# Optimization experiments

Measured on AMD Instinct MI355X. Metric: run time of the kernel, lower is better.

## Reference

```python
import jax, jax.numpy as jnp
import numpy as np

N = 50000          # node_num
E = 800000         # edges before self-loops (avg degree 16)
H = 1              # heads
C = 64             # out_channel (== embedding dim)
D_IN = 64          # in_channel
NEG_SLOPE = 0.2    # GraphLayer leaky_relu negative_slope
BN_EPS = 1e-5


def setup_inputs() -> dict:
    key = jax.random.key(0)
    ks = jax.random.split(key, 12)
    x = jax.random.normal(ks[0], (N, D_IN), jnp.float32)
    # random edges with no self-loops (forward removes then re-adds self-loops)
    src = jax.random.randint(ks[1], (E,), 0, N, dtype=jnp.int32)
    off = jax.random.randint(ks[2], (E,), 1, N, dtype=jnp.int32)
    dst = (src + off) % N
    edge_index = jnp.stack([src, dst])            # [2, E], row0=j (source), row1=i (target)
    embedding = jax.random.normal(ks[3], (N, C), jnp.float32)
    sc = 1.0 / np.sqrt(D_IN)
    W = jax.random.normal(ks[4], (H * C, D_IN), jnp.float32) * sc   # lin.weight
    att_i = jax.random.normal(ks[5], (1, H, C), jnp.float32) * 0.1
    att_j = jax.random.normal(ks[6], (1, H, C), jnp.float32) * 0.1
    att_em_i = jax.random.normal(ks[7], (1, H, C), jnp.float32) * 0.1
    att_em_j = jax.random.normal(ks[8], (1, H, C), jnp.float32) * 0.1
    bias = jnp.zeros((C,), jnp.float32)           # GraphLayer bias (concat=False)
    bn_gamma = jnp.ones((C,), jnp.float32)
    bn_beta = jnp.zeros((C,), jnp.float32)
    return {"x": x, "edge_index": edge_index, "embedding": embedding, "W": W,
            "att_i": att_i, "att_j": att_j, "att_em_i": att_em_i, "att_em_j": att_em_j,
            "bias": bias, "bn_gamma": bn_gamma, "bn_beta": bn_beta}


def reference(x, edge_index, embedding, W, att_i, att_j, att_em_i, att_em_j, bias, bn_gamma, bn_beta):
    n = x.shape[0]
    xl = (x @ W.T).reshape(n, H, C)                       # lin(x) -> [N, H, C]
    # add self-loops (input edges have none)
    loops = jnp.arange(n, dtype=edge_index.dtype)
    src = jnp.concatenate([edge_index[0], loops])         # j
    dst = jnp.concatenate([edge_index[1], loops])         # i (aggregation target)
    x_j = xl[src]                                         # [E', H, C]
    x_i = xl[dst]
    emb_i = embedding[dst][:, None, :]                    # [E', 1, C] broadcast over heads
    emb_j = embedding[src][:, None, :]
    # alpha = <cat(x_i, emb_i), cat(att_i, att_em_i)> + <cat(x_j, emb_j), cat(att_j, att_em_j)>
    a = ((x_i * att_i).sum(-1) + (emb_i * att_em_i).sum(-1)
         + (x_j * att_j).sum(-1) + (emb_j * att_em_j).sum(-1))   # [E', H]
    a = jnp.where(a >= 0, a, NEG_SLOPE * a)               # leaky_relu(0.2)
    # segment softmax over target nodes
    amax = jax.ops.segment_max(a, dst, num_segments=n)    # every node has a self-loop
    ea = jnp.exp(a - amax[dst])
    denom = jax.ops.segment_sum(ea, dst, num_segments=n)
    alpha = ea / (denom[dst] + 1e-16)                     # [E', H]
    msg = x_j * alpha[..., None]                          # [E', H, C]
    out = jax.ops.segment_sum(msg, dst, num_segments=n)   # [N, H, C]
    out = out.mean(axis=1) + bias                         # concat=False -> head mean
    # BatchNorm1d (training mode: batch stats) + ReLU
    mu = out.mean(axis=0)
    var = ((out - mu) ** 2).mean(axis=0)
    out = (out - mu) * jax.lax.rsqrt(var + BN_EPS) * bn_gamma + bn_beta
    return jnp.maximum(out, 0.0)
```

## Files before the change

### kernel.cpp

```cpp
#include <hip/hip_runtime.h>
#include <hip/hip_bf16.h>

#define NEG_SLOPE 0.2f
#define BN_EPS 1e-5f
#define CAP 48
#define OWNMAX 768

typedef __attribute__((ext_vector_type(8))) short bf16x8;
typedef __attribute__((ext_vector_type(4))) float f32x4;

__device__ __forceinline__ bf16x8 pk8(float4 a, float4 b) {
    union { __hip_bfloat16 h; short s; } u;
    bf16x8 r;
    u.h = __float2bfloat16(a.x); r[0] = u.s;
    u.h = __float2bfloat16(a.y); r[1] = u.s;
    u.h = __float2bfloat16(a.z); r[2] = u.s;
    u.h = __float2bfloat16(a.w); r[3] = u.s;
    u.h = __float2bfloat16(b.x); r[4] = u.s;
    u.h = __float2bfloat16(b.y); r[5] = u.s;
    u.h = __float2bfloat16(b.z); r[6] = u.s;
    u.h = __float2bfloat16(b.w); r[7] = u.s;
    return r;
}

__global__ void __launch_bounds__(256, 4)
k_scatter_mfma(const float* __restrict__ x, const float* __restrict__ W,
               const float* __restrict__ emb,
               const float* __restrict__ att_i, const float* __restrict__ att_j,
               const float* __restrict__ att_em_i, const float* __restrict__ att_em_j,
               const int* __restrict__ src, const int* __restrict__ dst, int E,
               int* __restrict__ cursor, unsigned short* __restrict__ bucket,
               __hip_bfloat16* __restrict__ xlh, float* __restrict__ s_i,
               float* __restrict__ s_j, int N) {
    __shared__ int nown;
    __shared__ int ownidx[OWNMAX];
    {
        int myx = blockIdx.x & 7;
        int slice = blockIdx.x >> 3;
        int per = (E + 255) / 256;
        int e0 = slice * per;
        int e1 = e0 + per; if (e1 > E) e1 = E;
        if (threadIdx.x == 0) nown = 0;
        __syncthreads();
        for (int e = e0 + threadIdx.x; e < e1; e += 256) {
            int d = dst[e];
            if (((d >> 6) & 7) == myx) {
                int k = atomicAdd(&nown, 1);
                if (k < OWNMAX) ownidx[k] = e;
            }
        }
        __syncthreads();
        int n = nown < OWNMAX ? nown : OWNMAX;
        for (int k = threadIdx.x; k < n; k += 256) {
            int e = ownidx[k];
            int d = dst[e];
            int p = atomicAdd(&cursor[d], 1);
            if (p < CAP) bucket[(size_t)d * CAP + p] = (unsigned short)src[e];
        }
    }

    int gw = blockIdx.x * 4 + (threadIdx.x >> 6);
    int ntiles = (N + 15) >> 4;
    if (gw >= ntiles) return;
    int lane = threadIdx.x & 63;
    int m = lane & 15;
    int q = lane >> 4;
    int r0 = gw * 16;

    const float* xrow = x + (size_t)(r0 + m) * 64;
    float4 xa0 = *(const float4*)(xrow + q * 8);
    float4 xa1 = *(const float4*)(xrow + q * 8 + 4);
    float4 xb0 = *(const float4*)(xrow + 32 + q * 8);
    float4 xb1 = *(const float4*)(xrow + 32 + q * 8 + 4);
    bf16x8 A0 = pk8(xa0, xa1);
    bf16x8 A1 = pk8(xb0, xb1);

    f32x4 acc0 = {0.f, 0.f, 0.f, 0.f}, acc1 = acc0, acc2 = acc0, acc3 = acc0;
#define CTILE(ct, accv) { \
        const float* wrow = W + (size_t)(ct * 16 + m) * 64; \
        float4 wb0 = *(const float4*)(wrow + q * 8); \
        float4 wb1 = *(const float4*)(wrow + q * 8 + 4); \
        float4 wb2 = *(const float4*)(wrow + 32 + q * 8); \
        float4 wb3 = *(const float4*)(wrow + 32 + q * 8 + 4); \
        bf16x8 B0 = pk8(wb0, wb1); \
        bf16x8 B1 = pk8(wb2, wb3); \
        accv = __builtin_amdgcn_mfma_f32_16x16x32_bf16(A0, B0, accv, 0, 0, 0); \
        accv = __builtin_amdgcn_mfma_f32_16x16x32_bf16(A1, B1, accv, 0, 0, 0); }
    CTILE(0, acc0) CTILE(1, acc1) CTILE(2, acc2) CTILE(3, acc3)
#undef CTILE

    float ati0 = att_i[m],    ati1 = att_i[16 + m],    ati2 = att_i[32 + m],    ati3 = att_i[48 + m];
    float atj0 = att_j[m],    atj1 = att_j[16 + m],    atj2 = att_j[32 + m],    atj3 = att_j[48 + m];
    float aei0 = att_em_i[m], aei1 = att_em_i[16 + m], aei2 = att_em_i[32 + m], aei3 = att_em_i[48 + m];
    float aej0 = att_em_j[m], aej1 = att_em_j[16 + m], aej2 = att_em_j[32 + m], aej3 = att_em_j[48 + m];
#pragma unroll
    for (int reg = 0; reg < 4; ++reg) {
        int r = r0 + q * 4 + reg;
        if (r < N) {
            float v0 = acc0[reg], v1 = acc1[reg], v2 = acc2[reg], v3 = acc3[reg];
            __hip_bfloat16* xo = xlh + (size_t)r * 64 + m;
            xo[0]  = __float2bfloat16(v0);
            xo[16] = __float2bfloat16(v1);
            xo[32] = __float2bfloat16(v2);
            xo[48] = __float2bfloat16(v3);
            const float* er = emb + (size_t)r * 64 + m;
            float e0 = er[0], e1 = er[16], e2 = er[32], e3 = er[48];
            float pi = v0 * ati0 + v1 * ati1 + v2 * ati2 + v3 * ati3
                     + e0 * aei0 + e1 * aei1 + e2 * aei2 + e3 * aei3;
            float pj = v0 * atj0 + v1 * atj1 + v2 * atj2 + v3 * atj3
                     + e0 * aej0 + e1 * aej1 + e2 * aej2 + e3 * aej3;
#pragma unroll
            for (int o = 1; o < 16; o <<= 1) {
                pi += __shfl_xor(pi, o, 64);
                pj += __shfl_xor(pj, o, 64);
            }
            if (m == 0) { s_i[r] = pi; s_j[r] = pj; }
        }
    }
}

__global__ void __launch_bounds__(256, 8)
k_aggregate(const __hip_bfloat16* __restrict__ xlh, const float* __restrict__ s_i,
            const float* __restrict__ s_j, const int* __restrict__ cursor,
            const unsigned short* __restrict__ bucket, const float* __restrict__ bias,
            __hip_bfloat16* __restrict__ preh, int N) {
    int lane = threadIdx.x & 63;
    int w = threadIdx.x >> 6;
    int i = blockIdx.x * 4 + w;
    if (i >= N) return;

    int deg = cursor[i];
    deg = deg < CAP ? deg : CAP;
    size_t base = (size_t)i * CAP;
    float sii = s_i[i];
    float a_self = sii + s_j[i];
    a_self = a_self >= 0.f ? a_self : NEG_SLOPE * a_self;

    int jreg = 0;
    float areg = -1e30f;
    if (lane < deg) {
        jreg = (int)bucket[base + lane];
        float a = sii + s_j[jreg];
        areg = a >= 0.f ? a : NEG_SLOPE * a;
    }
    float mx = fmaxf(a_self, areg);
#pragma unroll
    for (int o = 32; o; o >>= 1) mx = fmaxf(mx, __shfl_xor(mx, o, 64));
    float wreg = (lane < deg) ? __expf(areg - mx) : 0.f;
    float dsum = wreg;
#pragma unroll
    for (int o = 32; o; o >>= 1) dsum += __shfl_xor(dsum, o, 64);
    float w_self = __expf(a_self - mx);
    float denom = dsum + w_self + 1e-16f;

    float acc = w_self * (float)xlh[(size_t)i * 64 + lane];
    int wbits = __float_as_int(wreg);
    int e = 0;
#define GL(k) int j##k = __builtin_amdgcn_readlane(jreg, e + k); \
              float u##k = __int_as_float(__builtin_amdgcn_readlane(wbits, e + k)); \
              float v##k = (float)xlh[(size_t)j##k * 64 + lane];
#define FM(k) acc = fmaf(u##k, v##k, acc);
    for (; e + 15 < deg; e += 16) {
        GL(0) GL(1) GL(2) GL(3) GL(4) GL(5) GL(6) GL(7)
        GL(8) GL(9) GL(10) GL(11) GL(12) GL(13) GL(14) GL(15)
        FM(0) FM(1) FM(2) FM(3) FM(4) FM(5) FM(6) FM(7)
        FM(8) FM(9) FM(10) FM(11) FM(12) FM(13) FM(14) FM(15)
    }
    for (; e + 7 < deg; e += 8) {
        GL(0) GL(1) GL(2) GL(3) GL(4) GL(5) GL(6) GL(7)
        FM(0) FM(1) FM(2) FM(3) FM(4) FM(5) FM(6) FM(7)
    }
#undef GL
#undef FM
    for (; e < deg; ++e) {
        int j = __builtin_amdgcn_readlane(jreg, e);
        float wv = __int_as_float(__builtin_amdgcn_readlane(wbits, e));
        acc = fmaf(wv, (float)xlh[(size_t)j * 64 + lane], acc);
    }
    preh[(size_t)i * 64 + lane] = __float2bfloat16(acc / denom + bias[lane]);
}

__global__ void k_stats(const __hip_bfloat16* __restrict__ preh, int N,
                        float* __restrict__ sums) {
    int lane = threadIdx.x & 63, w = threadIdx.x >> 6;
    int gwave = blockIdx.x * (blockDim.x >> 6) + w;
    int stride = gridDim.x * (blockDim.x >> 6);
    float s = 0.f, q = 0.f;
    for (int r = gwave; r < N; r += stride) {
        float v = (float)preh[(size_t)r * 64 + lane];
        s += v;
        q = fmaf(v, v, q);
    }
    __shared__ float ls[4][64], lq[4][64];
    ls[w][lane] = s;
    lq[w][lane] = q;
    __syncthreads();
    if (w == 0) {
        s = ls[0][lane] + ls[1][lane] + ls[2][lane] + ls[3][lane];
        q = lq[0][lane] + lq[1][lane] + lq[2][lane] + lq[3][lane];
        atomicAdd(&sums[lane], s);
        atomicAdd(&sums[64 + lane], q);
    }
}

__global__ void __launch_bounds__(256, 4)
k_norm(const __hip_bfloat16* __restrict__ preh, const float* __restrict__ sums,
       const float* __restrict__ gamma, const float* __restrict__ beta,
       float* __restrict__ out, int N, int total4) {
    __shared__ float sc_sh[64], sh_sh[64];
    int tid = threadIdx.x;
    if (tid < 64) {
        float invN = 1.f / (float)N;
        float mu = sums[tid] * invN;
        float var = sums[64 + tid] * invN - mu * mu;
        float sc = gamma[tid] * rsqrtf(var + BN_EPS);
        sc_sh[tid] = sc;
        sh_sh[tid] = beta[tid] - mu * sc;
    }
    __syncthreads();
    typedef __attribute__((ext_vector_type(4))) short s16x4;
    union { s16x4 v; short s[4]; } u;
    for (int i = blockIdx.x * blockDim.x + tid; i < total4; i += gridDim.x * blockDim.x) {
        int c = (i & 15) * 4;
        u.v = ((const s16x4*)preh)[i];
        float4 r;
        union { __hip_bfloat16 h; short s; } cv;
        cv.s = u.s[0]; r.x = fmaxf(fmaf((float)cv.h, sc_sh[c + 0], sh_sh[c + 0]), 0.f);
        cv.s = u.s[1]; r.y = fmaxf(fmaf((float)cv.h, sc_sh[c + 1], sh_sh[c + 1]), 0.f);
        cv.s = u.s[2]; r.z = fmaxf(fmaf((float)cv.h, sc_sh[c + 2], sh_sh[c + 2]), 0.f);
        cv.s = u.s[3]; r.w = fmaxf(fmaf((float)cv.h, sc_sh[c + 3], sh_sh[c + 3]), 0.f);
        ((float4*)out)[i] = r;
    }
}

extern "C" void kernel_launch(void* const* d_in, const int* in_sizes, int n_in,
                              void* d_out, int out_size, void* d_ws, size_t ws_size,
                              hipStream_t stream) {
    const float* x        = (const float*)d_in[0];
    const int*   ei       = (const int*)d_in[1];
    const float* emb      = (const float*)d_in[2];
    const float* W        = (const float*)d_in[3];
    const float* att_i    = (const float*)d_in[4];
    const float* att_j    = (const float*)d_in[5];
    const float* att_em_i = (const float*)d_in[6];
    const float* att_em_j = (const float*)d_in[7];
    const float* bias     = (const float*)d_in[8];
    const float* gamma    = (const float*)d_in[9];
    const float* beta     = (const float*)d_in[10];

    int N = in_sizes[0] / 64;
    int E = in_sizes[1] / 2;
    const int* srcv = ei;
    const int* dstv = ei + E;

    char* ws = (char*)d_ws;
    size_t o = 0;
    auto alloc = [&](size_t bytes) -> char* {
        char* p = ws + o;
        o += bytes;
        o = (o + 255) & ~(size_t)255;
        return p;
    };
    __hip_bfloat16* xlh    = (__hip_bfloat16*)alloc((size_t)N * 64 * 2);
    __hip_bfloat16* preh   = (__hip_bfloat16*)alloc((size_t)N * 64 * 2);
    float* s_i             = (float*)alloc((size_t)N * 4);
    float* s_j             = (float*)alloc((size_t)N * 4);
    unsigned short* bucket = (unsigned short*)alloc((size_t)N * CAP * 2);
    char*  zbase  = alloc((size_t)N * 4 + 128 * 4);
    int*   cursor = (int*)zbase;
    float* sums   = (float*)(zbase + (size_t)N * 4);

    hipMemsetAsync(zbase, 0, (size_t)N * 4 + 128 * 4, stream);

    k_scatter_mfma<<<2048, 256, 0, stream>>>(x, W, emb, att_i, att_j, att_em_i,
                                             att_em_j, srcv, dstv, E, cursor, bucket,
                                             xlh, s_i, s_j, N);
    k_aggregate<<<(N + 3) / 4, 256, 0, stream>>>(xlh, s_i, s_j, cursor, bucket,
                                                 bias, preh, N);
    k_stats<<<256, 256, 0, stream>>>(preh, N, sums);
    int total4 = N * 16;
    k_norm<<<512, 256, 0, stream>>>(preh, sums, gamma, beta, (float*)d_out, N, total4);
}
```

Measured before the change: 190.1 us.

## Vectorize edge bucketing, cache dst in LDS, swizzle aggregate blocks across XCDs

New measurement: 179.7 us. 1.06x faster.

```diff
diff --git a/kernel.cpp b/kernel.cpp
--- a/kernel.cpp
+++ b/kernel.cpp
@@ -23,7 +23,7 @@
     return r;
 }
 
-__global__ void __launch_bounds__(256, 4)
+__global__ void __launch_bounds__(256, 8)
 k_scatter_mfma(const float* __restrict__ x, const float* __restrict__ W,
                const float* __restrict__ emb,
                const float* __restrict__ att_i, const float* __restrict__ att_j,
@@ -34,35 +34,63 @@
                float* __restrict__ s_j, int N) {
     __shared__ int nown;
     __shared__ int ownidx[OWNMAX];
+    __shared__ int owndst[OWNMAX];
+    int tid = threadIdx.x;
     {
         int myx = blockIdx.x & 7;
         int slice = blockIdx.x >> 3;
-        int per = (E + 255) / 256;
+        int per = ((E + 255) >> 8);
+        per = (per + 3) & ~3;
         int e0 = slice * per;
         int e1 = e0 + per; if (e1 > E) e1 = E;
-        if (threadIdx.x == 0) nown = 0;
+        if (tid == 0) nown = 0;
         __syncthreads();
-        for (int e = e0 + threadIdx.x; e < e1; e += 256) {
-            int d = dst[e];
-            if (((d >> 6) & 7) == myx) {
-                int k = atomicAdd(&nown, 1);
-                if (k < OWNMAX) ownidx[k] = e;
+        if (e0 < e1) {
+            int e1a = e0 + ((e1 - e0) & ~3);
+#define APP(dd, ee) if ((((dd) >> 6) & 7) == myx) { \
+            int k_ = atomicAdd(&nown, 1); \
+            if (k_ < OWNMAX) { ownidx[k_] = (ee); owndst[k_] = (dd); } }
+            for (int e = e0 + tid * 4; e < e1a; e += 1024) {
+                int4 d4 = *(const int4*)(dst + e);
+                APP(d4.x, e)
+                APP(d4.y, e + 1)
+                APP(d4.z, e + 2)
+                APP(d4.w, e + 3)
             }
+            for (int e = e1a + tid; e < e1; e += 256) {
+                int d = dst[e];
+                APP(d, e)
+            }
+#undef APP
         }
         __syncthreads();
         int n = nown < OWNMAX ? nown : OWNMAX;
-        for (int k = threadIdx.x; k < n; k += 256) {
+        int k0 = tid, k1 = tid + 256;
+        bool v0 = k0 < n, v1 = k1 < n;
+        int ea = v0 ? ownidx[k0] : 0, da = v0 ? owndst[k0] : 0;
+        int eb = v1 ? ownidx[k1] : 0, db = v1 ? owndst[k1] : 0;
+        int sa = v0 ? src[ea] : 0;
+        int sb = v1 ? src[eb] : 0;
+        if (v0) {
+            int p = atomicAdd(&cursor[da], 1);
+            if (p < CAP) bucket[(size_t)da * CAP + p] = (unsigned short)sa;
+        }
+        if (v1) {
+            int p = atomicAdd(&cursor[db], 1);
+            if (p < CAP) bucket[(size_t)db * CAP + p] = (unsigned short)sb;
+        }
+        for (int k = tid + 512; k < n; k += 256) {
             int e = ownidx[k];
-            int d = dst[e];
+            int d = owndst[k];
             int p = atomicAdd(&cursor[d], 1);
             if (p < CAP) bucket[(size_t)d * CAP + p] = (unsigned short)src[e];
         }
     }
 
-    int gw = blockIdx.x * 4 + (threadIdx.x >> 6);
+    int gw = blockIdx.x * 4 + (tid >> 6);
     int ntiles = (N + 15) >> 4;
     if (gw >= ntiles) return;
-    int lane = threadIdx.x & 63;
+    int lane = tid & 63;
     int m = lane & 15;
     int q = lane >> 4;
     int r0 = gw * 16;
@@ -126,23 +154,28 @@
             __hip_bfloat16* __restrict__ preh, int N) {
     int lane = threadIdx.x & 63;
     int w = threadIdx.x >> 6;
-    int i = blockIdx.x * 4 + w;
+    int blk = blockIdx.x;
+    int t = blk >> 3;
+    int g = ((t >> 4) << 7) + ((blk & 7) << 4) + (t & 15);
+    int i = g * 4 + w;
     if (i >= N) return;
 
     int deg = cursor[i];
     deg = deg < CAP ? deg : CAP;
     size_t base = (size_t)i * CAP;
     float sii = s_i[i];
-    float a_self = sii + s_j[i];
-    a_self = a_self >= 0.f ? a_self : NEG_SLOPE * a_self;
-
+    float sji = s_j[i];
+    float selfx = (float)xlh[(size_t)i * 64 + lane];
+    float bi = bias[lane];
     int jreg = 0;
+    if (lane < deg) jreg = (int)bucket[base + lane];
     float areg = -1e30f;
     if (lane < deg) {
-        jreg = (int)bucket[base + lane];
         float a = sii + s_j[jreg];
         areg = a >= 0.f ? a : NEG_SLOPE * a;
     }
+    float a_self = sii + sji;
+    a_self = a_self >= 0.f ? a_self : NEG_SLOPE * a_self;
     float mx = fmaxf(a_self, areg);
 #pragma unroll
     for (int o = 32; o; o >>= 1) mx = fmaxf(mx, __shfl_xor(mx, o, 64));
@@ -153,31 +186,23 @@
     float w_self = __expf(a_self - mx);
     float denom = dsum + w_self + 1e-16f;
 
-    float acc = w_self * (float)xlh[(size_t)i * 64 + lane];
+    float acc = w_self * selfx;
     int wbits = __float_as_int(wreg);
-    int e = 0;
+    int nb = (deg + 15) >> 4;
 #define GL(k) int j##k = __builtin_amdgcn_readlane(jreg, e + k); \
               float u##k = __int_as_float(__builtin_amdgcn_readlane(wbits, e + k)); \
               float v##k = (float)xlh[(size_t)j##k * 64 + lane];
 #define FM(k) acc = fmaf(u##k, v##k, acc);
-    for (; e + 15 < deg; e += 16) {
+    for (int b = 0; b < nb; ++b) {
+        int e = b << 4;
         GL(0) GL(1) GL(2) GL(3) GL(4) GL(5) GL(6) GL(7)
         GL(8) GL(9) GL(10) GL(11) GL(12) GL(13) GL(14) GL(15)
         FM(0) FM(1) FM(2) FM(3) FM(4) FM(5) FM(6) FM(7)
         FM(8) FM(9) FM(10) FM(11) FM(12) FM(13) FM(14) FM(15)
     }
-    for (; e + 7 < deg; e += 8) {
-        GL(0) GL(1) GL(2) GL(3) GL(4) GL(5) GL(6) GL(7)
-        FM(0) FM(1) FM(2) FM(3) FM(4) FM(5) FM(6) FM(7)
-    }
 #undef GL
 #undef FM
-    for (; e < deg; ++e) {
-        int j = __builtin_amdgcn_readlane(jreg, e);
-        float wv = __int_as_float(__builtin_amdgcn_readlane(wbits, e));
-        acc = fmaf(wv, (float)xlh[(size_t)j * 64 + lane], acc);
-    }
-    preh[(size_t)i * 64 + lane] = __float2bfloat16(acc / denom + bias[lane]);
+    preh[(size_t)i * 64 + lane] = __float2bfloat16(acc / denom + bi);
 }
 
 __global__ void k_stats(const __hip_bfloat16* __restrict__ preh, int N,
@@ -275,8 +300,9 @@
     k_scatter_mfma<<<2048, 256, 0, stream>>>(x, W, emb, att_i, att_j, att_em_i,
                                              att_em_j, srcv, dstv, E, cursor, bucket,
                                              xlh, s_i, s_j, N);
-    k_aggregate<<<(N + 3) / 4, 256, 0, stream>>>(xlh, s_i, s_j, cursor, bucket,
-                                                 bias, preh, N);
+    int nblk2 = (((N + 3) / 4) + 127) & ~127;
+    k_aggregate<<<nblk2, 256, 0, stream>>>(xlh, s_i, s_j, cursor, bucket,
+                                           bias, preh, N);
     k_stats<<<256, 256, 0, stream>>>(preh, N, sums);
     int total4 = N * 16;
     k_norm<<<512, 256, 0, stream>>>(preh, sums, gamma, beta, (float*)d_out, N, total4);
```
